# Performance work log

Hardware: AMD Instinct MI355X
Metric: run time of the kernel (lower is better)

Reference implementation:

```python
import jax, jax.numpy as jnp
import numpy as np

B, D_IN, D_PROJ, N_CLS = 4096, 4096, 1024, 32
N_CHILD = (32, 64)


def setup_inputs() -> dict:
    key = jax.random.key(0)
    ks = jax.random.split(key, 12)
    std = 2e-05
    inp = {
        "x": jax.random.normal(ks[0], (B, D_IN), dtype=jnp.float32),
        "y": jax.random.randint(ks[1], (B,), 0, N_CLS, dtype=jnp.int32),
        # parent projection: Linear(D_IN, D_PROJ)
        "Wp": jax.random.normal(ks[2], (D_IN, D_PROJ), dtype=jnp.float32) * std,
        "bp": jnp.zeros((D_PROJ,), jnp.float32),
        # subclass projection: Linear(D_IN, D_PROJ)
        "Ws": jax.random.normal(ks[3], (D_IN, D_PROJ), dtype=jnp.float32) * std,
        "bs": jnp.zeros((D_PROJ,), jnp.float32),
        # parent classifier: Linear(D_PROJ, N_CLS)
        "Wc": jax.random.normal(ks[4], (D_PROJ, N_CLS), dtype=jnp.float32) * std,
        "bc": jnp.zeros((N_CLS,), jnp.float32),
        # child expert banks: level i has N_CLS experts of Linear(D_PROJ, N_CHILD[i])
        "cw0": jax.random.normal(ks[5], (N_CLS, N_CHILD[0], D_PROJ), dtype=jnp.float32) * std,
        "cb0": jnp.zeros((N_CLS, N_CHILD[0]), jnp.float32),
        "cw1": jax.random.normal(ks[6], (N_CLS, N_CHILD[1], D_PROJ), dtype=jnp.float32) * std,
        "cb1": jnp.zeros((N_CLS, N_CHILD[1]), jnp.float32),
    }
    return inp


def reference(x, y, Wp, bp, Ws, bs, Wc, bc, cw0, cb0, cw1, cb1):
    # dropout p = 0.0 -> identity
    parent_proj_embed = x @ Wp + bp                 # [B, D_PROJ]
    parent_logits = parent_proj_embed @ Wc + bc     # [B, N_CLS]
    child_proj_embed = x @ Ws + bs                  # [B, D_PROJ]
    # per-sample expert routing: gather the expert for label y[b], then batched matvec
    child_logits0 = jnp.einsum("bd,bnd->bn", child_proj_embed, cw0[y]) + cb0[y]  # [B, 32]
    child_logits1 = jnp.einsum("bd,bnd->bn", child_proj_embed, cw1[y]) + cb1[y]  # [B, 64]
    return (parent_logits, child_logits0, child_logits1, parent_proj_embed, child_proj_embed)
```

## Files before the change

### kernel.cpp

```cpp
#include <hip/hip_runtime.h>
#include <hip/hip_bf16.h>
#include <stdint.h>


typedef __attribute__((ext_vector_type(4))) float  floatx4;
typedef __attribute__((ext_vector_type(8))) short  shortx8;
typedef __attribute__((ext_vector_type(4))) short  shortx4;
typedef __attribute__((ext_vector_type(8))) __bf16 bf16x8;

static __device__ __forceinline__ ushort f32_to_bf16_rne(float f) {
  uint32_t u = __builtin_bit_cast(uint32_t, f);
  u += 0x7FFFu + ((u >> 16) & 1u);
  return (ushort)(u >> 16);
}

static __device__ __forceinline__ void async_copy16(const void* g, void* lds) {
  __builtin_amdgcn_global_load_lds(
      (__attribute__((address_space(1))) void*)(uintptr_t)g,
      (__attribute__((address_space(3))) void*)(uintptr_t)lds,
      16, 0, 0);
}

__global__ __launch_bounds__(256) void k_prep(
    const float* __restrict__ x,   const int* __restrict__ y,
    const float* __restrict__ Wp,  const float* __restrict__ Ws,
    const float* __restrict__ Wc,
    const float* __restrict__ cw0, const float* __restrict__ cw1,
    ushort* __restrict__ xb,  ushort* __restrict__ Bt1,
    ushort* __restrict__ cwb, ushort* __restrict__ Wcb,
    int* __restrict__ perm, int* __restrict__ offs,
    int* __restrict__ work, int* __restrict__ nwork)
{
  __shared__ __align__(16) ushort tile[64 * 72];
  __shared__ int hist[32], hbase[32], hcur[32];
  const int b = blockIdx.x;
  const int t = threadIdx.x;

  if (b == 0) {
    if (t < 32) { hist[t] = 0; hcur[t] = 0; }
    __syncthreads();
    int yv[16];
    #pragma unroll
    for (int i = 0; i < 16; ++i) { yv[i] = y[t * 16 + i]; atomicAdd(&hist[yv[i]], 1); }
    __syncthreads();
    if (t == 0) {
      int s = 0;
      for (int c = 0; c < 32; ++c) { hbase[c] = s; offs[c] = s; s += hist[c]; }
      offs[32] = s;
      int nw = 0;
      for (int m = 0; m < 32; ++m) work[nw++] = (32 << 8) | m;
      for (int c = 0; c < 32; ++c)
        for (int m0 = 0; m0 < hist[c]; m0 += 128) work[nw++] = (c << 8) | (m0 >> 7);
      nwork[0] = nw;
    }
    __syncthreads();
    #pragma unroll
    for (int i = 0; i < 16; ++i) {
      const int c = yv[i];
      const int p = atomicAdd(&hcur[c], 1);
      perm[hbase[c] + p] = t * 16 + i;
    }
  } else if (b <= 4224) {
    const int row = b - 1;
    const int k = t * 4;
    float v0 = 0.f, v1 = 0.f, v2 = 0.f, v3 = 0.f;
    ushort* dst;
    if (row < 4096) {
      const int c = row >> 7, n = row & 127;
      if (n < 32) {
        floatx4 f = *reinterpret_cast<const floatx4*>(cw0 + (size_t)(c * 32 + n) * 1024 + k);
        v0 = f[0]; v1 = f[1]; v2 = f[2]; v3 = f[3];
      } else if (n < 96) {
        floatx4 f = *reinterpret_cast<const floatx4*>(cw1 + (size_t)(c * 64 + (n - 32)) * 1024 + k);
        v0 = f[0]; v1 = f[1]; v2 = f[2]; v3 = f[3];
      }
      dst = cwb + (size_t)row * 1024 + k;
    } else {
      const int n = row - 4096;
      if (n < 32) {
        v0 = Wc[(k + 0) * 32 + n]; v1 = Wc[(k + 1) * 32 + n];
        v2 = Wc[(k + 2) * 32 + n]; v3 = Wc[(k + 3) * 32 + n];
      }
      dst = Wcb + (size_t)n * 1024 + k;
    }
    shortx4 o;
    o[0] = (short)f32_to_bf16_rne(v0); o[1] = (short)f32_to_bf16_rne(v1);
    o[2] = (short)f32_to_bf16_rne(v2); o[3] = (short)f32_to_bf16_rne(v3);
    *reinterpret_cast<shortx4*>(dst) = o;
  } else if (b <= 6272) {
    const int vt = b - 4225;
    const int z = vt >> 10, rest = vt & 1023;
    const int nt = rest >> 6, kt = rest & 63;
    const float* W = z ? Ws : Wp;
    const int r = t >> 4, c = (t & 15) * 4;
    #pragma unroll
    for (int j = 0; j < 4; ++j) {
      const int kk = r + j * 16;
      floatx4 v = *reinterpret_cast<const floatx4*>(
          W + (size_t)(kt * 64 + kk) * 1024 + nt * 64 + c);
      tile[(c + 0) * 72 + kk] = f32_to_bf16_rne(v[0]);
      tile[(c + 1) * 72 + kk] = f32_to_bf16_rne(v[1]);
      tile[(c + 2) * 72 + kk] = f32_to_bf16_rne(v[2]);
      tile[(c + 3) * 72 + kk] = f32_to_bf16_rne(v[3]);
    }
    __syncthreads();
    const int nl = t >> 3, ch = t & 7;
    #pragma unroll
    for (int j = 0; j < 2; ++j) {
      const int n = nl + j * 32;
      shortx8 v = *reinterpret_cast<const shortx8*>(tile + n * 72 + ch * 8);
      *reinterpret_cast<shortx8*>(
          Bt1 + (size_t)(z * 1024 + nt * 64 + n) * 4096 + kt * 64 + ch * 8) = v;
    }
  } else {
    const size_t i = ((size_t)(b - 6273) * 256 + t) * 8;
    floatx4 a = *reinterpret_cast<const floatx4*>(x + i);
    floatx4 c = *reinterpret_cast<const floatx4*>(x + i + 4);
    shortx8 o;
    o[0] = (short)f32_to_bf16_rne(a[0]); o[1] = (short)f32_to_bf16_rne(a[1]);
    o[2] = (short)f32_to_bf16_rne(a[2]); o[3] = (short)f32_to_bf16_rne(a[3]);
    o[4] = (short)f32_to_bf16_rne(c[0]); o[5] = (short)f32_to_bf16_rne(c[1]);
    o[6] = (short)f32_to_bf16_rne(c[2]); o[7] = (short)f32_to_bf16_rne(c[3]);
    *reinterpret_cast<shortx8*>(xb + i) = o;
  }
}

__global__ __launch_bounds__(512, 2) void k_gemm1(
    const ushort* __restrict__ xb, const ushort* __restrict__ Bt1,
    const float* __restrict__ bp, const float* __restrict__ bs,
    float* __restrict__ outP, float* __restrict__ outS,
    ushort* __restrict__ Pb, ushort* __restrict__ Sb)
{
  __shared__ __align__(16) ushort lA[3 * 256 * 64];
  __shared__ __align__(16) ushort lB[3 * 128 * 64];

  floatx4 acc[4][4];
  const floatx4 z4 = {0.f, 0.f, 0.f, 0.f};
  #pragma unroll
  for (int i = 0; i < 4; ++i)
    #pragma unroll
    for (int j = 0; j < 4; ++j) acc[i][j] = z4;

  const int t    = threadIdx.x;
  const int w    = t >> 6;
  const int lane = t & 63;
  const int wr   = w >> 1;
  const int wc   = w & 1;
  const int r16  = lane & 15;
  const int qd   = lane >> 4;

  const ushort* Abase = xb  + (size_t)(blockIdx.x * 256) * 4096;
  const ushort* Bbase = Bt1 + (size_t)(blockIdx.y * 128) * 4096;

  const int    rS   = t >> 3;
  const int    qs   = ((t & 7) ^ (rS & 7)) << 3;
  const int    dUni = (t & ~63) * 8;

  const int px0 = (0 * 4 + qd) ^ (r16 & 7);
  const int px1 = (1 * 4 + qd) ^ (r16 & 7);
  const int aRd = (wr * 64 + r16) * 64;
  const int bRd = (wc * 64 + r16) * 64;

  #define STAGE_CHUNK(slot, k0)                                                \
    do {                                                                       \
      _Pragma("unroll")                                                        \
      for (int j = 0; j < 4; ++j)                                              \
        async_copy16(Abase + (size_t)(j * 64 + rS) * 4096 + (k0) + qs,         \
                     lA + (slot) * 16384 + j * 4096 + dUni);                   \
      _Pragma("unroll")                                                        \
      for (int j = 0; j < 2; ++j)                                              \
        async_copy16(Bbase + (size_t)(j * 64 + rS) * 4096 + (k0) + qs,         \
                     lB + (slot) * 8192 + j * 4096 + dUni);                    \
    } while (0)

  STAGE_CHUNK(0, 0);
  STAGE_CHUNK(1, 64);
  asm volatile("s_waitcnt vmcnt(6)" ::: "memory");
  __builtin_amdgcn_s_barrier();
  asm volatile("" ::: "memory");

  for (int c = 0; c < 64; ++c) {
    const int slot = c % 3;
    const ushort* As = lA + slot * 16384;
    const ushort* Bs = lB + slot * 8192;

    bf16x8 af[2][4], bfv[2][4];
    #pragma unroll
    for (int mi = 0; mi < 4; ++mi) {
      af[0][mi] = *reinterpret_cast<const bf16x8*>(As + aRd + mi * 1024 + px0 * 8);
      af[1][mi] = *reinterpret_cast<const bf16x8*>(As + aRd + mi * 1024 + px1 * 8);
    }
    #pragma unroll
    for (int ni = 0; ni < 4; ++ni) {
      bfv[0][ni] = *reinterpret_cast<const bf16x8*>(Bs + bRd + ni * 1024 + px0 * 8);
      bfv[1][ni] = *reinterpret_cast<const bf16x8*>(Bs + bRd + ni * 1024 + px1 * 8);
    }

    {
      const int cs  = c + 2;
      const int ss  = cs % 3;
      const int k0s = (cs < 64 ? cs : 63) * 64;
      STAGE_CHUNK(ss, k0s);
    }

    __builtin_amdgcn_s_setprio(1);
    #pragma unroll
    for (int ks = 0; ks < 2; ++ks)
      #pragma unroll
      for (int mi = 0; mi < 4; ++mi)
        #pragma unroll
        for (int ni = 0; ni < 4; ++ni)
          acc[mi][ni] = __builtin_amdgcn_mfma_f32_16x16x32_bf16(
              af[ks][mi], bfv[ks][ni], acc[mi][ni], 0, 0, 0);
    __builtin_amdgcn_s_setprio(0);

    asm volatile("s_waitcnt vmcnt(6)" ::: "memory");
    __builtin_amdgcn_s_barrier();
    asm volatile("" ::: "memory");
  }
  #undef STAGE_CHUNK

  const int sel = (blockIdx.y >= 8);
  const float* bias = sel ? bs : bp;
  float*  outF = sel ? outS : outP;
  ushort* outB = sel ? Sb : Pb;
  const int colbase = blockIdx.y * 128 - sel * 1024;
  #pragma unroll
  for (int mi = 0; mi < 4; ++mi) {
    #pragma unroll
    for (int ni = 0; ni < 4; ++ni) {
      const int n = colbase + wc * 64 + ni * 16 + r16;
      const float bv = bias[n];
      #pragma unroll
      for (int rg = 0; rg < 4; ++rg) {
        const int m = blockIdx.x * 256 + wr * 64 + mi * 16 + qd * 4 + rg;
        const float v = acc[mi][ni][rg] + bv;
        const size_t off = (size_t)m * 1024 + n;
        outF[off] = v;
        outB[off] = f32_to_bf16_rne(v);
      }
    }
  }
}

static __device__ __forceinline__ void load_frags64(
    const ushort* lA, const ushort* lB, bf16x8 af[2][4], bf16x8 bfv[2][4],
    int wr, int wc, int r16, int quad)
{
  #pragma unroll
  for (int ks = 0; ks < 2; ++ks) {
    const int pc = (((ks * 4) + quad) ^ (r16 & 7)) * 8;
    #pragma unroll
    for (int mi = 0; mi < 4; ++mi)
      af[ks][mi] = *reinterpret_cast<const bf16x8*>(lA + (wr * 64 + mi * 16 + r16) * 64 + pc);
    #pragma unroll
    for (int ni = 0; ni < 4; ++ni)
      bfv[ks][ni] = *reinterpret_cast<const bf16x8*>(lB + (wc * 64 + ni * 16 + r16) * 64 + pc);
  }
}

static __device__ __forceinline__ void mfma_frags64(
    bf16x8 af[2][4], bf16x8 bfv[2][4], floatx4 acc[4][4])
{
  __builtin_amdgcn_s_setprio(1);
  #pragma unroll
  for (int ks = 0; ks < 2; ++ks)
    #pragma unroll
    for (int mi = 0; mi < 4; ++mi)
      #pragma unroll
      for (int ni = 0; ni < 4; ++ni)
        acc[mi][ni] = __builtin_amdgcn_mfma_f32_16x16x32_bf16(
            af[ks][mi], bfv[ks][ni], acc[mi][ni], 0, 0, 0);
  __builtin_amdgcn_s_setprio(0);
}

__global__ __launch_bounds__(256) void k_head(
    const ushort* __restrict__ Sb, const ushort* __restrict__ Pb,
    const ushort* __restrict__ cwb, const ushort* __restrict__ Wcb,
    const int* __restrict__ perm, const int* __restrict__ off,
    const int* __restrict__ work, const int* __restrict__ nwork,
    const float* __restrict__ cb0, const float* __restrict__ cb1,
    const float* __restrict__ bc,
    float* __restrict__ out0, float* __restrict__ out1,
    float* __restrict__ outParent)
{
  __shared__ __align__(16) ushort lA[4 * 128 * 64];
  __shared__ __align__(16) ushort lB[4 * 128 * 64];

  const int t = threadIdx.x, w = t >> 6, lane = t & 63;
  const int wr = w >> 1, wc = w & 1, r16 = lane & 15, quad = lane >> 4;
  const int sr = lane >> 3, sc = lane & 7;
  const int gc = sc ^ sr;
  const int dRow = 32 * w;
  const int nW = nwork[0];

  for (int wi = blockIdx.x; wi < nW; wi += 96) {
    const int item = work[wi];
    const int cls  = item >> 8;
    const int mt   = item & 255;

    floatx4 acc[4][4];
    const floatx4 z4 = {0.f, 0.f, 0.f, 0.f};
    #pragma unroll
    for (int i = 0; i < 4; ++i)
      #pragma unroll
      for (int j = 0; j < 4; ++j) acc[i][j] = z4;

    int off0 = 0, cnt = 0;
    const ushort* Asrc;
    const ushort* Bb;
    int rowG[4];
    if (cls == 32) {
      Asrc = Pb;
      Bb   = Wcb;
      #pragma unroll
      for (int c2 = 0; c2 < 4; ++c2) rowG[c2] = mt * 128 + dRow + 8 * c2 + sr;
    } else {
      off0 = off[cls];
      cnt  = off[cls + 1] - off0;
      Asrc = Sb;
      Bb   = cwb + (size_t)cls * 128 * 1024;
      #pragma unroll
      for (int c2 = 0; c2 < 4; ++c2) {
        const int r = mt * 128 + dRow + 8 * c2 + sr;
        rowG[c2] = perm[off0 + min(r, cnt - 1)];
      }
    }

    #define STAGE_H(slot, k0)                                                  \
      do {                                                                     \
        _Pragma("unroll")                                                      \
        for (int c2 = 0; c2 < 4; ++c2) {                                       \
          async_copy16(Asrc + (size_t)rowG[c2] * 1024 + (k0) + gc * 8,         \
                       lA + (slot) * 8192 + (dRow + 8 * c2) * 64);             \
          async_copy16(Bb + (size_t)(dRow + 8 * c2 + sr) * 1024 + (k0) + gc * 8,\
                       lB + (slot) * 8192 + (dRow + 8 * c2) * 64);             \
        }                                                                      \
      } while (0)

    STAGE_H(0, 0);
    STAGE_H(1, 64);
    STAGE_H(2, 128);
    asm volatile("s_waitcnt vmcnt(16)" ::: "memory");
    __builtin_amdgcn_s_barrier();
    asm volatile("" ::: "memory");

    for (int c = 0; c < 16; ++c) {
      const int slot = c & 3;
      bf16x8 af[2][4], bfv[2][4];
      load_frags64(lA + slot * 8192, lB + slot * 8192, af, bfv, wr, wc, r16, quad);
      {
        const int cs  = c + 3;
        const int ss  = cs & 3;
        const int k0s = (cs < 16 ? cs : 15) * 64;
        STAGE_H(ss, k0s);
      }
      mfma_frags64(af, bfv, acc);
      asm volatile("s_waitcnt vmcnt(16)" ::: "memory");
      __builtin_amdgcn_s_barrier();
      asm volatile("" ::: "memory");
    }
    #undef STAGE_H

    if (cls == 32) {
      if (wc == 0) {
        #pragma unroll
        for (int mi = 0; mi < 4; ++mi)
          #pragma unroll
          for (int ni = 0; ni < 2; ++ni) {
            const int n = ni * 16 + r16;
            const float bv = bc[n];
            #pragma unroll
            for (int rg = 0; rg < 4; ++rg) {
              const int m = mt * 128 + wr * 64 + mi * 16 + quad * 4 + rg;
              outParent[(size_t)m * 32 + n] = acc[mi][ni][rg] + bv;
            }
          }
      }
    } else {
      const int m0 = mt * 128;
      #pragma unroll
      for (int mi = 0; mi < 4; ++mi) {
        #pragma unroll
        for (int rg = 0; rg < 4; ++rg) {
          const int gm = m0 + wr * 64 + mi * 16 + quad * 4 + rg;
          if (gm >= cnt) continue;
          const int sample = perm[off0 + gm];
          #pragma unroll
          for (int ni = 0; ni < 4; ++ni) {
            const int n = wc * 64 + ni * 16 + r16;
            if (n < 32)
              out0[(size_t)sample * 32 + n] = acc[mi][ni][rg] + cb0[cls * 32 + n];
            else if (n < 96)
              out1[(size_t)sample * 64 + (n - 32)] = acc[mi][ni][rg] + cb1[cls * 64 + (n - 32)];
          }
        }
      }
    }
  }
}


extern "C" void kernel_launch(void* const* d_in, const int* in_sizes, int n_in,
                              void* d_out, int out_size, void* d_ws, size_t ws_size,
                              hipStream_t stream) {
  const float* x   = (const float*)d_in[0];
  const int*   y   = (const int*)  d_in[1];
  const float* Wp  = (const float*)d_in[2];
  const float* bp  = (const float*)d_in[3];
  const float* Ws  = (const float*)d_in[4];
  const float* bs  = (const float*)d_in[5];
  const float* Wc  = (const float*)d_in[6];
  const float* bc  = (const float*)d_in[7];
  const float* cw0 = (const float*)d_in[8];
  const float* cb0 = (const float*)d_in[9];
  const float* cw1 = (const float*)d_in[10];
  const float* cb1 = (const float*)d_in[11];

  float* out = (float*)d_out;
  float* parent_logits = out;
  float* child0        = out + 131072;
  float* child1        = out + 262144;
  float* P             = out + 524288;
  float* S             = out + 4718592;

  char* ws = (char*)d_ws;
  ushort* xb   = (ushort*)(ws);
  ushort* Bt1  = (ushort*)(ws + 33554432);
  ushort* Pb   = (ushort*)(ws + 50331648);
  ushort* Sb   = (ushort*)(ws + 58720256);
  ushort* cwb  = (ushort*)(ws + 67108864);
  ushort* Wcb  = (ushort*)(ws + 75497472);
  int*    perm = (int*)   (ws + 75759616);
  int*    offs = (int*)   (ws + 75776000);
  int*    work = (int*)   (ws + 75776256);
  int*    nwk  = (int*)   (ws + 75776768);

  k_prep <<<14465, 256, 0, stream>>>(x, y, Wp, Ws, Wc, cw0, cw1,
                                     xb, Bt1, cwb, Wcb, perm, offs, work, nwk);
  k_gemm1<<<dim3(16, 16), 512, 0, stream>>>(xb, Bt1, bp, bs, P, S, Pb, Sb);
  k_head <<<96, 256, 0, stream>>>(Sb, Pb, cwb, Wcb, perm, offs, work, nwk,
                                  cb0, cb1, bc,
                                  child0, child1, parent_logits);
}
```

Baseline: 248.2 us.

## Fuse x fp32-to-bf16 conversion into GEMM A-tile loading

Removes the separate x conversion pass from the prep kernel. The GEMM now loads fp32 x into registers, converts it with packed bf16 conversion instructions and writes it to LDS, double-buffering the registers across chunks. This avoids writing and re-reading a 32MB bf16 copy of x. The cost is that A traffic inside the GEMM doubles (fp32 instead of bf16), each x tile is re-read by all 16 column blocks, and register pressure plus extra VALU and LDS-write work rise in the main loop.

```diff
diff --git a/kernel.cpp b/kernel.cpp
--- a/kernel.cpp
+++ b/kernel.cpp
@@ -3,15 +3,22 @@
 #include <stdint.h>
 
 
-typedef __attribute__((ext_vector_type(4))) float  floatx4;
-typedef __attribute__((ext_vector_type(8))) short  shortx8;
-typedef __attribute__((ext_vector_type(4))) short  shortx4;
-typedef __attribute__((ext_vector_type(8))) __bf16 bf16x8;
+typedef __attribute__((ext_vector_type(4))) float    floatx4;
+typedef __attribute__((ext_vector_type(8))) short    shortx8;
+typedef __attribute__((ext_vector_type(4))) short    shortx4;
+typedef __attribute__((ext_vector_type(4))) uint32_t uintx4;
+typedef __attribute__((ext_vector_type(8))) __bf16   bf16x8;
 
 static __device__ __forceinline__ ushort f32_to_bf16_rne(float f) {
   uint32_t u = __builtin_bit_cast(uint32_t, f);
   u += 0x7FFFu + ((u >> 16) & 1u);
   return (ushort)(u >> 16);
+}
+
+static __device__ __forceinline__ uint32_t cvt_pk_bf16(float lo, float hi) {
+  uint32_t r;
+  asm("v_cvt_pk_bf16_f32 %0, %1, %2" : "=v"(r) : "v"(lo), "v"(hi));
+  return r;
 }
 
 static __device__ __forceinline__ void async_copy16(const void* g, void* lds) {
@@ -22,11 +29,11 @@
 }
 
 __global__ __launch_bounds__(256) void k_prep(
-    const float* __restrict__ x,   const int* __restrict__ y,
+    const int* __restrict__ y,
     const float* __restrict__ Wp,  const float* __restrict__ Ws,
     const float* __restrict__ Wc,
     const float* __restrict__ cw0, const float* __restrict__ cw1,
-    ushort* __restrict__ xb,  ushort* __restrict__ Bt1,
+    ushort* __restrict__ Bt1,
     ushort* __restrict__ cwb, ushort* __restrict__ Wcb,
     int* __restrict__ perm, int* __restrict__ offs,
     int* __restrict__ work, int* __restrict__ nwork)
@@ -87,7 +94,7 @@
     o[0] = (short)f32_to_bf16_rne(v0); o[1] = (short)f32_to_bf16_rne(v1);
     o[2] = (short)f32_to_bf16_rne(v2); o[3] = (short)f32_to_bf16_rne(v3);
     *reinterpret_cast<shortx4*>(dst) = o;
-  } else if (b <= 6272) {
+  } else {
     const int vt = b - 4225;
     const int z = vt >> 10, rest = vt & 1023;
     const int nt = rest >> 6, kt = rest & 63;
@@ -112,21 +119,11 @@
       *reinterpret_cast<shortx8*>(
           Bt1 + (size_t)(z * 1024 + nt * 64 + n) * 4096 + kt * 64 + ch * 8) = v;
     }
-  } else {
-    const size_t i = ((size_t)(b - 6273) * 256 + t) * 8;
-    floatx4 a = *reinterpret_cast<const floatx4*>(x + i);
-    floatx4 c = *reinterpret_cast<const floatx4*>(x + i + 4);
-    shortx8 o;
-    o[0] = (short)f32_to_bf16_rne(a[0]); o[1] = (short)f32_to_bf16_rne(a[1]);
-    o[2] = (short)f32_to_bf16_rne(a[2]); o[3] = (short)f32_to_bf16_rne(a[3]);
-    o[4] = (short)f32_to_bf16_rne(c[0]); o[5] = (short)f32_to_bf16_rne(c[1]);
-    o[6] = (short)f32_to_bf16_rne(c[2]); o[7] = (short)f32_to_bf16_rne(c[3]);
-    *reinterpret_cast<shortx8*>(xb + i) = o;
   }
 }
 
 __global__ __launch_bounds__(512, 2) void k_gemm1(
-    const ushort* __restrict__ xb, const ushort* __restrict__ Bt1,
+    const float* __restrict__ x, const ushort* __restrict__ Bt1,
     const float* __restrict__ bp, const float* __restrict__ bs,
     float* __restrict__ outP, float* __restrict__ outS,
     ushort* __restrict__ Pb, ushort* __restrict__ Sb)
@@ -149,76 +146,116 @@
   const int r16  = lane & 15;
   const int qd   = lane >> 4;
 
-  const ushort* Abase = xb  + (size_t)(blockIdx.x * 256) * 4096;
+  const float*  Ax    = x   + (size_t)(blockIdx.x * 256) * 4096;
   const ushort* Bbase = Bt1 + (size_t)(blockIdx.y * 128) * 4096;
 
-  const int    rS   = t >> 3;
-  const int    qs   = ((t & 7) ^ (rS & 7)) << 3;
-  const int    dUni = (t & ~63) * 8;
+  const int rS   = t >> 3;
+  const int pA   = t & 7;
+  const int q    = pA ^ (rS & 7);
+  const int qf   = q << 3;
+  const int qsB  = q << 3;
+  const int dUni = (t & ~63) * 8;
+
+  const float* aSrc0 = Ax + (size_t)(0 * 64 + rS) * 4096 + qf;
+  const float* aSrc1 = Ax + (size_t)(1 * 64 + rS) * 4096 + qf;
+  const float* aSrc2 = Ax + (size_t)(2 * 64 + rS) * 4096 + qf;
+  const float* aSrc3 = Ax + (size_t)(3 * 64 + rS) * 4096 + qf;
 
   const int px0 = (0 * 4 + qd) ^ (r16 & 7);
   const int px1 = (1 * 4 + qd) ^ (r16 & 7);
   const int aRd = (wr * 64 + r16) * 64;
   const int bRd = (wc * 64 + r16) * 64;
 
-  #define STAGE_CHUNK(slot, k0)                                                \
-    do {                                                                       \
-      _Pragma("unroll")                                                        \
-      for (int j = 0; j < 4; ++j)                                              \
-        async_copy16(Abase + (size_t)(j * 64 + rS) * 4096 + (k0) + qs,         \
-                     lA + (slot) * 16384 + j * 4096 + dUni);                   \
-      _Pragma("unroll")                                                        \
-      for (int j = 0; j < 2; ++j)                                              \
-        async_copy16(Bbase + (size_t)(j * 64 + rS) * 4096 + (k0) + qs,         \
-                     lB + (slot) * 8192 + j * 4096 + dUni);                    \
+  floatx4 aEv[8], aOd[8];
+
+  #define STAGE_B(slot, k0)                                                  \
+    do {                                                                     \
+      async_copy16(Bbase + (size_t)(0 * 64 + rS) * 4096 + (k0) + qsB,        \
+                   lB + (slot) * 8192 + 0 * 4096 + dUni);                    \
+      async_copy16(Bbase + (size_t)(1 * 64 + rS) * 4096 + (k0) + qsB,        \
+                   lB + (slot) * 8192 + 1 * 4096 + dUni);                    \
     } while (0)
 
-  STAGE_CHUNK(0, 0);
-  STAGE_CHUNK(1, 64);
-  asm volatile("s_waitcnt vmcnt(6)" ::: "memory");
+  #define LOAD_A(reg, k0)                                                    \
+    do {                                                                     \
+      reg[0] = *reinterpret_cast<const floatx4*>(aSrc0 + (k0));              \
+      reg[1] = *reinterpret_cast<const floatx4*>(aSrc0 + (k0) + 4);          \
+      reg[2] = *reinterpret_cast<const floatx4*>(aSrc1 + (k0));              \
+      reg[3] = *reinterpret_cast<const floatx4*>(aSrc1 + (k0) + 4);          \
+      reg[4] = *reinterpret_cast<const floatx4*>(aSrc2 + (k0));              \
+      reg[5] = *reinterpret_cast<const floatx4*>(aSrc2 + (k0) + 4);          \
+      reg[6] = *reinterpret_cast<const floatx4*>(aSrc3 + (k0));              \
+      reg[7] = *reinterpret_cast<const floatx4*>(aSrc3 + (k0) + 4);          \
+    } while (0)
+
+  #define WRITE_A(reg, slot)                                                 \
+    do {                                                                     \
+      _Pragma("unroll")                                                      \
+      for (int j = 0; j < 4; ++j) {                                          \
+        uintx4 o;                                                            \
+        o[0] = cvt_pk_bf16(reg[2*j][0],   reg[2*j][1]);                      \
+        o[1] = cvt_pk_bf16(reg[2*j][2],   reg[2*j][3]);                      \
+        o[2] = cvt_pk_bf16(reg[2*j+1][0], reg[2*j+1][1]);                    \
+        o[3] = cvt_pk_bf16(reg[2*j+1][2], reg[2*j+1][3]);                    \
+        *reinterpret_cast<uintx4*>(                                          \
+            lA + (slot) * 16384 + (j * 64 + rS) * 64 + pA * 8) = o;          \
+      }                                                                      \
+    } while (0)
+
+  STAGE_B(0, 0);   LOAD_A(aEv, 0);
+  STAGE_B(1, 64);  LOAD_A(aOd, 64);
+  asm volatile("s_waitcnt vmcnt(10)" ::: "memory");
+  WRITE_A(aEv, 0);
+  asm volatile("s_waitcnt lgkmcnt(0)" ::: "memory");
   __builtin_amdgcn_s_barrier();
   asm volatile("" ::: "memory");
 
-  for (int c = 0; c < 64; ++c) {
-    const int slot = c % 3;
-    const ushort* As = lA + slot * 16384;
-    const ushort* Bs = lB + slot * 8192;
-
-    bf16x8 af[2][4], bfv[2][4];
-    #pragma unroll
-    for (int mi = 0; mi < 4; ++mi) {
-      af[0][mi] = *reinterpret_cast<const bf16x8*>(As + aRd + mi * 1024 + px0 * 8);
-      af[1][mi] = *reinterpret_cast<const bf16x8*>(As + aRd + mi * 1024 + px1 * 8);
-    }
-    #pragma unroll
-    for (int ni = 0; ni < 4; ++ni) {
-      bfv[0][ni] = *reinterpret_cast<const bf16x8*>(Bs + bRd + ni * 1024 + px0 * 8);
-      bfv[1][ni] = *reinterpret_cast<const bf16x8*>(Bs + bRd + ni * 1024 + px1 * 8);
-    }
-
-    {
-      const int cs  = c + 2;
-      const int ss  = cs % 3;
-      const int k0s = (cs < 64 ? cs : 63) * 64;
-      STAGE_CHUNK(ss, k0s);
-    }
-
-    __builtin_amdgcn_s_setprio(1);
-    #pragma unroll
-    for (int ks = 0; ks < 2; ++ks)
-      #pragma unroll
-      for (int mi = 0; mi < 4; ++mi)
-        #pragma unroll
-        for (int ni = 0; ni < 4; ++ni)
-          acc[mi][ni] = __builtin_amdgcn_mfma_f32_16x16x32_bf16(
-              af[ks][mi], bfv[ks][ni], acc[mi][ni], 0, 0, 0);
-    __builtin_amdgcn_s_setprio(0);
-
-    asm volatile("s_waitcnt vmcnt(6)" ::: "memory");
-    __builtin_amdgcn_s_barrier();
-    asm volatile("" ::: "memory");
+  #define CHUNK_BODY(c, regIssue, regWrite)                                  \
+    do {                                                                     \
+      const int slot = (c) % 3;                                              \
+      const ushort* As = lA + slot * 16384;                                  \
+      const ushort* Bs = lB + slot * 8192;                                   \
+      bf16x8 af[2][4], bfv[2][4];                                            \
+      _Pragma("unroll")                                                      \
+      for (int mi = 0; mi < 4; ++mi) {                                       \
+        af[0][mi] = *reinterpret_cast<const bf16x8*>(As + aRd + mi * 1024 + px0 * 8); \
+        af[1][mi] = *reinterpret_cast<const bf16x8*>(As + aRd + mi * 1024 + px1 * 8); \
+      }                                                                      \
+      _Pragma("unroll")                                                      \
+      for (int ni = 0; ni < 4; ++ni) {                                       \
+        bfv[0][ni] = *reinterpret_cast<const bf16x8*>(Bs + bRd + ni * 1024 + px0 * 8); \
+        bfv[1][ni] = *reinterpret_cast<const bf16x8*>(Bs + bRd + ni * 1024 + px1 * 8); \
+      }                                                                      \
+      const int cs  = (c) + 2;                                               \
+      const int ss  = cs % 3;                                                \
+      const int k0s = (cs < 64 ? cs : 63) * 64;                              \
+      STAGE_B(ss, k0s);                                                      \
+      LOAD_A(regIssue, k0s);                                                 \
+      __builtin_amdgcn_s_setprio(1);                                         \
+      _Pragma("unroll")                                                      \
+      for (int ks = 0; ks < 2; ++ks)                                         \
+        _Pragma("unroll")                                                    \
+        for (int mi = 0; mi < 4; ++mi)                                       \
+          _Pragma("unroll")                                                  \
+          for (int ni = 0; ni < 4; ++ni)                                     \
+            acc[mi][ni] = __builtin_amdgcn_mfma_f32_16x16x32_bf16(           \
+                af[ks][mi], bfv[ks][ni], acc[mi][ni], 0, 0, 0);              \
+      __builtin_amdgcn_s_setprio(0);                                         \
+      asm volatile("s_waitcnt vmcnt(10)" ::: "memory");                      \
+      WRITE_A(regWrite, ((c) + 1) % 3);                                      \
+      asm volatile("s_waitcnt lgkmcnt(0)" ::: "memory");                     \
+      __builtin_amdgcn_s_barrier();                                          \
+      asm volatile("" ::: "memory");                                         \
+    } while (0)
+
+  for (int c = 0; c < 64; c += 2) {
+    CHUNK_BODY(c,     aEv, aOd);
+    CHUNK_BODY(c + 1, aOd, aEv);
   }
-  #undef STAGE_CHUNK
+  #undef CHUNK_BODY
+  #undef STAGE_B
+  #undef LOAD_A
+  #undef WRITE_A
 
   const int sel = (blockIdx.y >= 8);
   const float* bias = sel ? bs : bp;
@@ -425,7 +462,6 @@
   float* S             = out + 4718592;
 
   char* ws = (char*)d_ws;
-  ushort* xb   = (ushort*)(ws);
   ushort* Bt1  = (ushort*)(ws + 33554432);
   ushort* Pb   = (ushort*)(ws + 50331648);
   ushort* Sb   = (ushort*)(ws + 58720256);
@@ -436,9 +472,9 @@
   int*    work = (int*)   (ws + 75776256);
   int*    nwk  = (int*)   (ws + 75776768);
 
-  k_prep <<<14465, 256, 0, stream>>>(x, y, Wp, Ws, Wc, cw0, cw1,
-                                     xb, Bt1, cwb, Wcb, perm, offs, work, nwk);
-  k_gemm1<<<dim3(16, 16), 512, 0, stream>>>(xb, Bt1, bp, bs, P, S, Pb, Sb);
+  k_prep <<<6273, 256, 0, stream>>>(y, Wp, Ws, Wc, cw0, cw1,
+                                    Bt1, cwb, Wcb, perm, offs, work, nwk);
+  k_gemm1<<<dim3(16, 16), 512, 0, stream>>>(x, Bt1, bp, bs, P, S, Pb, Sb);
   k_head <<<96, 256, 0, stream>>>(Sb, Pb, cwb, Wcb, perm, offs, work, nwk,
                                   cb0, cb1, bc,
                                   child0, child1, parent_logits);
```

New measurement: 282.5 us. +13.8%, slower.
